# Kernel tuning notes

Measured on AMD Instinct MI355X. Metric: run time of the kernel, lower is better.

## Reference

```python
import jax, jax.numpy as jnp
import numpy as np

B, S, D, H = 8, 1024, 512, 8  # batch, seq_len, d_model (per-head!), num_heads


def setup_inputs() -> dict:
    key = jax.random.key(0)
    ks = jax.random.split(key, 9)
    q_ip = jax.random.normal(ks[0], (B, S, D), dtype=jnp.float32)
    k_ip = jax.random.normal(ks[1], (B, S, D), dtype=jnp.float32)
    v_ip = jax.random.normal(ks[2], (B, S, D), dtype=jnp.float32)
    # float padding-style mask, 1 => masked out (added as mask * -1e9)
    mask = (jax.random.uniform(ks[3], (B, 1, S, S)) < 0.1).astype(jnp.float32)
    scale = 1.0 / np.sqrt(D)  # lecun_normal-ish init scale
    wq = jax.random.normal(ks[4], (D, D * H), dtype=jnp.float32) * scale
    wk = jax.random.normal(ks[5], (D, D * H), dtype=jnp.float32) * scale
    wv = jax.random.normal(ks[6], (D, D * H), dtype=jnp.float32) * scale
    wo = jax.random.normal(ks[7], (D * H, D), dtype=jnp.float32) * (1.0 / np.sqrt(D * H))
    bq = jnp.zeros((D * H,), jnp.float32)
    bk = jnp.zeros((D * H,), jnp.float32)
    bv = jnp.zeros((D * H,), jnp.float32)
    bo = jnp.zeros((D,), jnp.float32)
    return {"v_ip": v_ip, "k_ip": k_ip, "q_ip": q_ip, "mask": mask,
            "wq": wq, "bq": bq, "wk": wk, "bk": bk, "wv": wv, "bv": bv,
            "wo": wo, "bo": bo}


def _split_heads(x, batch, heads, depth):
    # (B, S, H*D) -> (B, H, S, D)
    return x.reshape(batch, -1, heads, depth).transpose(0, 2, 1, 3)


def reference(v_ip, k_ip, q_ip, mask, wq, bq, wk, bk, wv, bv, wo, bo):
    batch = q_ip.shape[0]
    depth = q_ip.shape[-1]          # d_model (= per-head depth in this 'narrow' MHA)
    heads = wq.shape[-1] // depth
    q = _split_heads(q_ip @ wq + bq, batch, heads, depth)  # (B,H,Sq,D)
    k = _split_heads(k_ip @ wk + bk, batch, heads, depth)  # (B,H,Sk,D)
    v = _split_heads(v_ip @ wv + bv, batch, heads, depth)  # (B,H,Sk,D)
    logits = jnp.einsum('bhqd,bhkd->bhqk', q, k) / jnp.sqrt(jnp.float32(depth))
    logits = logits + mask * (-1e9)
    attn = jax.nn.softmax(logits, axis=-1)                  # (B,H,Sq,Sk)
    ctx = jnp.einsum('bhqk,bhkd->bhqd', attn, v)
    ctx = ctx.transpose(0, 2, 1, 3).reshape(batch, -1, heads * depth)
    out = ctx @ wo + bo                                     # (B,Sq,d_model)
    return out, attn
```

## Files before the change

### kernel.cpp

```cpp
#include <hip/hip_runtime.h>
#include <stdint.h>
#include <stddef.h>

typedef _Float16 h16;
typedef __attribute__((ext_vector_type(4))) _Float16 h16x4;
typedef __attribute__((ext_vector_type(8))) _Float16 h16x8;
typedef __attribute__((ext_vector_type(4))) float f32x4;

#define MFMA16(a, b, c) __builtin_amdgcn_mfma_f32_16x16x32_f16((a), (b), (c), 0, 0, 0)

#define NB 8
#define SEQ 1024
#define DEP 512
#define NH 8
#define HD 4096
#define BS 8192

static __device__ __forceinline__ void gload_lds16(const void* g, void* l) {
  __builtin_amdgcn_global_load_lds((__attribute__((address_space(1))) void*)(g),
                                   (__attribute__((address_space(3))) void*)(l),
                                   16, 0, 0);
}

static __device__ __forceinline__ h16 f2h(float f) { return (h16)f; }

__global__ __launch_bounds__(256) void k_conv3(const float* __restrict__ q,
                                               const float* __restrict__ k,
                                               const float* __restrict__ v,
                                               h16* __restrict__ xq, h16* __restrict__ xk,
                                               h16* __restrict__ xv) {
  int z = blockIdx.y;
  const float* in = z == 0 ? q : (z == 1 ? k : v);
  h16* out = z == 0 ? xq : (z == 1 ? xk : xv);
  int i = blockIdx.x * 256 + threadIdx.x;
  float4 f = ((const float4*)in)[i];
  h16x4 o = { f2h(f.x), f2h(f.y), f2h(f.z), f2h(f.w) };
  ((h16x4*)out)[i] = o;
}

__global__ __launch_bounds__(256) void k_maskbits(const float* __restrict__ mask,
                                                  uint32_t* __restrict__ bits) {
  int g = blockIdx.x * 256 + threadIdx.x;
  const float4* mp = (const float4*)mask + (size_t)g * 8;
  uint32_t w = 0;
#pragma unroll
  for (int u = 0; u < 8; ++u) {
    float4 f = mp[u];
    w |= (f.x != 0.f ? 1u : 0u) << (u * 4);
    w |= (f.y != 0.f ? 1u : 0u) << (u * 4 + 1);
    w |= (f.z != 0.f ? 1u : 0u) << (u * 4 + 2);
    w |= (f.w != 0.f ? 1u : 0u) << (u * 4 + 3);
  }
  bits[g] = w;
}

__global__ __launch_bounds__(256) void k_transpose(const float* __restrict__ in,
                                                   h16* __restrict__ out, int R, int C) {
  __shared__ float t[32][33];
  int c0 = blockIdx.x * 32, r0 = blockIdx.y * 32;
  int tx = threadIdx.x & 31, ty = threadIdx.x >> 5;
  for (int p = 0; p < 4; ++p)
    t[ty + p * 8][tx] = in[(size_t)(r0 + ty + p * 8) * C + c0 + tx];
  __syncthreads();
  for (int p = 0; p < 4; ++p)
    out[(size_t)(c0 + ty + p * 8) * R + r0 + tx] = f2h(t[tx][ty + p * 8]);
}

__global__ __launch_bounds__(256) void k_transpose3(const float* __restrict__ wq,
                                                    const float* __restrict__ wk,
                                                    const float* __restrict__ wv,
                                                    h16* __restrict__ oq, h16* __restrict__ ok,
                                                    h16* __restrict__ ov) {
  __shared__ float t[32][33];
  int z = blockIdx.z;
  const float* in = z == 0 ? wq : (z == 1 ? wk : wv);
  h16* out = z == 0 ? oq : (z == 1 ? ok : ov);
  const int R = 512, C = 4096;
  int c0 = blockIdx.x * 32, r0 = blockIdx.y * 32;
  int tx = threadIdx.x & 31, ty = threadIdx.x >> 5;
  for (int p = 0; p < 4; ++p)
    t[ty + p * 8][tx] = in[(size_t)(r0 + ty + p * 8) * C + c0 + tx];
  __syncthreads();
  for (int p = 0; p < 4; ++p)
    out[(size_t)(c0 + ty + p * 8) * R + r0 + tx] = f2h(t[tx][ty + p * 8]);
}

__global__ __launch_bounds__(256) void k_gemm_qkv(
    const h16* __restrict__ xq, const h16* __restrict__ xk, const h16* __restrict__ xv,
    const h16* __restrict__ WqT, const h16* __restrict__ WkT, const h16* __restrict__ WvT,
    const float* __restrict__ bq, const float* __restrict__ bk, const float* __restrict__ bv,
    h16* __restrict__ Qh, h16* __restrict__ Kh, h16* __restrict__ Vt) {
  __shared__ __align__(16) h16 As[128 * 64];
  __shared__ __align__(16) h16 Bs[128 * 64];
  const int z = blockIdx.z;
  const h16* A = z == 0 ? xq : (z == 1 ? xk : xv);
  const h16* Bm = z == 0 ? WqT : (z == 1 ? WkT : WvT);
  const float* bias = z == 0 ? bq : (z == 1 ? bk : bv);
  const int K = 512;
  const int tid = threadIdx.x, lane = tid & 63, wave = tid >> 6;
  const int wm = (wave >> 1) * 64, wn = (wave & 1) * 64;
  const int m0 = blockIdx.y * 128;
  const int n0 = blockIdx.x * 128;

  f32x4 acc[4][4];
  for (int i = 0; i < 4; ++i)
    for (int j = 0; j < 4; ++j) acc[i][j] = (f32x4)0.0f;

  const int lrow = lane >> 3, lcol = (lane & 7) * 8;
  const int fr = lane & 15, qd = lane >> 4;

  for (int k0 = 0; k0 < K; k0 += 64) {
    __syncthreads();
    for (int i = 0; i < 4; ++i) {
      int g = wave * 4 + i;
      int row = g * 8 + lrow;
      gload_lds16(A + (size_t)(m0 + row) * K + k0 + lcol, As + g * 512);
      gload_lds16(Bm + (size_t)(n0 + row) * K + k0 + lcol, Bs + g * 512);
    }
    __syncthreads();
    for (int kk = 0; kk < 64; kk += 32) {
      h16x8 af[4], bf[4];
      for (int i = 0; i < 4; ++i)
        af[i] = *(const h16x8*)(As + (wm + i * 16 + fr) * 64 + kk + qd * 8);
      for (int j = 0; j < 4; ++j)
        bf[j] = *(const h16x8*)(Bs + (wn + j * 16 + fr) * 64 + kk + qd * 8);
      for (int i = 0; i < 4; ++i)
        for (int j = 0; j < 4; ++j) acc[i][j] = MFMA16(af[i], bf[j], acc[i][j]);
    }
  }

  h16* Cnat = z == 0 ? Qh : Kh;
  for (int i = 0; i < 4; ++i)
    for (int j = 0; j < 4; ++j) {
      int mbase = m0 + wm + i * 16 + qd * 4;
      int ncol = n0 + wn + j * 16 + fr;
      float bv2 = bias[ncol];
      if (z < 2) {
        for (int r = 0; r < 4; ++r)
          Cnat[(size_t)(mbase + r) * HD + ncol] = f2h(acc[i][j][r] + bv2);
      } else {
        int bb = mbase >> 10, ss = mbase & 1023;
        int hh = ncol >> 9, dd = ncol & 511;
        size_t addr = ((size_t)((bb * NH + hh) * DEP + dd)) * SEQ + ss;
        h16x4 pk = { f2h(acc[i][j][0] + bv2), f2h(acc[i][j][1] + bv2),
                     f2h(acc[i][j][2] + bv2), f2h(acc[i][j][3] + bv2) };
        *(h16x4*)(Vt + addr) = pk;
      }
    }
}

template <int OUT_MODE>
__global__ __launch_bounds__(256) void k_gemm_nt(const h16* __restrict__ A,
                                                 const h16* __restrict__ Bm,
                                                 const float* __restrict__ bias,
                                                 void* __restrict__ Cout,
                                                 int M, int N, int K, int ldc) {
  __shared__ __align__(16) h16 As[128 * 64];
  __shared__ __align__(16) h16 Bs[128 * 64];
  const int tid = threadIdx.x, lane = tid & 63, wave = tid >> 6;
  const int wm = (wave >> 1) * 64, wn = (wave & 1) * 64;
  const int m0 = blockIdx.y * 128;
  const int n0 = blockIdx.x * 128;

  f32x4 acc[4][4];
  for (int i = 0; i < 4; ++i)
    for (int j = 0; j < 4; ++j) acc[i][j] = (f32x4)0.0f;

  const int lrow = lane >> 3, lcol = (lane & 7) * 8;
  const int fr = lane & 15, qd = lane >> 4;

  for (int k0 = 0; k0 < K; k0 += 64) {
    __syncthreads();
    for (int i = 0; i < 4; ++i) {
      int g = wave * 4 + i;
      int row = g * 8 + lrow;
      gload_lds16(A + (size_t)(m0 + row) * K + k0 + lcol, As + g * 512);
      gload_lds16(Bm + (size_t)(n0 + row) * K + k0 + lcol, Bs + g * 512);
    }
    __syncthreads();
    for (int kk = 0; kk < 64; kk += 32) {
      h16x8 af[4], bf[4];
      for (int i = 0; i < 4; ++i)
        af[i] = *(const h16x8*)(As + (wm + i * 16 + fr) * 64 + kk + qd * 8);
      for (int j = 0; j < 4; ++j)
        bf[j] = *(const h16x8*)(Bs + (wn + j * 16 + fr) * 64 + kk + qd * 8);
      for (int i = 0; i < 4; ++i)
        for (int j = 0; j < 4; ++j) acc[i][j] = MFMA16(af[i], bf[j], acc[i][j]);
    }
  }

  for (int i = 0; i < 4; ++i)
    for (int j = 0; j < 4; ++j) {
      int mbase = m0 + wm + i * 16 + qd * 4;
      int ncol = n0 + wn + j * 16 + fr;
      float bv2 = bias ? bias[ncol] : 0.0f;
      float* Cp = (float*)Cout;
      for (int r = 0; r < 4; ++r)
        Cp[(size_t)(mbase + r) * ldc + ncol] = acc[i][j][r] + bv2;
    }
}

#define TQ 64
#define QS_LD 520
#define OFF_KS 66560
#define PA_C64 4616
#define OFF_RED 147712
#define CS_LD 536
#define SMEM_ATTN (OFF_RED + 2048)

__global__ __launch_bounds__(512, 2) void k_attn(const h16* __restrict__ Q,
                                                 const h16* __restrict__ Km,
                                                 const uint32_t* __restrict__ bits,
                                                 const h16* __restrict__ Vtg,
                                                 float* __restrict__ attn,
                                                 h16* __restrict__ ctx) {
  extern __shared__ __align__(16) char smem[];
  h16* Qs = (h16*)smem;
  h16* Ks = (h16*)(smem + OFF_KS);
  h16* Pa = (h16*)smem;
  h16* Cs = (h16*)smem;
  float* red = (float*)(smem + OFF_RED);

  const int tid = threadIdx.x, lane = tid & 63, wave = tid >> 6;
  const int qt = blockIdx.x, hh = blockIdx.y, b = blockIdx.z;
  const int q0 = qt * TQ;
  const int fr = lane & 15, qd = lane >> 4;
  const int ncol0 = wave * 128;
  const int bh = b * NH + hh;

  {
    const h16* Qg = Q + (size_t)(b * SEQ + q0) * HD + hh * DEP;
    for (int it = 0; it < 8; ++it) {
      int g = tid + it * 512;
      int row = g >> 6, c8 = g & 63;
      *(h16x8*)(Qs + row * QS_LD + c8 * 8) = *(const h16x8*)(Qg + (size_t)row * HD + c8 * 8);
    }
  }

  f32x4 acc[4][8];
  for (int i = 0; i < 4; ++i)
    for (int j = 0; j < 8; ++j) acc[i][j] = (f32x4)0.0f;

  for (int kc = 0; kc < 512; kc += 32) {
    __syncthreads();
    for (int c = 0; c < 8; ++c) {
      int nbase = wave * 128 + c * 16;
      int n = nbase + (lane >> 2);
      int s = lane & 3;
      int sp = (s - (n >> 1)) & 3;
      gload_lds16(Km + (size_t)(b * SEQ + n) * HD + hh * DEP + kc + sp * 8,
                  Ks + nbase * 32);
    }
    __syncthreads();
    h16x8 af[4];
    for (int i = 0; i < 4; ++i)
      af[i] = *(const h16x8*)(Qs + (i * 16 + fr) * QS_LD + kc + qd * 8);
#pragma unroll
    for (int j = 0; j < 8; ++j) {
      int n = ncol0 + j * 16 + fr;
      int slot = (qd + (n >> 1)) & 3;
      h16x8 bf = *(const h16x8*)(Ks + n * 32 + slot * 8);
      for (int i = 0; i < 4; ++i) acc[i][j] = MFMA16(af[i], bf, acc[i][j]);
    }
  }

  const float scale = 0.044194173824159216f;
  const uint32_t* bitp = bits + (size_t)(b * SEQ + q0) * 32 + wave * 4;
  float rmax[4][4];
#pragma unroll
  for (int i = 0; i < 4; ++i) {
    uint4 mwi[4];
    for (int r = 0; r < 4; ++r)
      mwi[r] = *(const uint4*)(bitp + (size_t)(i * 16 + qd * 4 + r) * 32);
    for (int r = 0; r < 4; ++r) rmax[i][r] = -3.4e38f;
#pragma unroll
    for (int j = 0; j < 8; ++j)
      for (int r = 0; r < 4; ++r) {
        uint32_t ww = (j >> 1) == 0 ? mwi[r].x
                    : (j >> 1) == 1 ? mwi[r].y
                    : (j >> 1) == 2 ? mwi[r].z : mwi[r].w;
        uint32_t m = (ww >> (fr + ((j & 1) << 4))) & 1u;
        float v = acc[i][j][r] * scale + (m ? -1e9f : 0.0f);
        acc[i][j][r] = v;
        rmax[i][r] = fmaxf(rmax[i][r], v);
      }
  }
  for (int i = 0; i < 4; ++i)
    for (int r = 0; r < 4; ++r)
      for (int off = 1; off < 16; off <<= 1)
        rmax[i][r] = fmaxf(rmax[i][r], __shfl_xor(rmax[i][r], off, 64));
  __syncthreads();
  if (fr == 0)
    for (int i = 0; i < 4; ++i)
      for (int r = 0; r < 4; ++r) red[wave * TQ + i * 16 + qd * 4 + r] = rmax[i][r];
  __syncthreads();
  float gmax[4][4];
  for (int i = 0; i < 4; ++i)
    for (int r = 0; r < 4; ++r) {
      int lr = i * 16 + qd * 4 + r;
      float m = red[lr];
      for (int w = 1; w < 8; ++w) m = fmaxf(m, red[w * TQ + lr]);
      gmax[i][r] = m;
    }
  __syncthreads();

  float rsum[4][4];
  for (int i = 0; i < 4; ++i)
    for (int r = 0; r < 4; ++r) rsum[i][r] = 0.f;
  for (int i = 0; i < 4; ++i)
    for (int j = 0; j < 8; ++j)
      for (int r = 0; r < 4; ++r) {
        float e = __expf(acc[i][j][r] - gmax[i][r]);
        acc[i][j][r] = e;
        rsum[i][r] += e;
      }
  for (int i = 0; i < 4; ++i)
    for (int r = 0; r < 4; ++r)
      for (int off = 1; off < 16; off <<= 1)
        rsum[i][r] += __shfl_xor(rsum[i][r], off, 64);
  if (fr == 0)
    for (int i = 0; i < 4; ++i)
      for (int r = 0; r < 4; ++r) red[wave * TQ + i * 16 + qd * 4 + r] = rsum[i][r];
  __syncthreads();

  for (int i = 0; i < 4; ++i)
    for (int r = 0; r < 4; ++r) {
      int lr = i * 16 + qd * 4 + r;
      float tot = 0.f;
      for (int w = 0; w < 8; ++w) tot += red[w * TQ + lr];
      float inv = 1.0f / tot;
#pragma unroll
      for (int j = 0; j < 8; ++j) {
        int c64 = wave * 2 + (j >> 2);
        int coff = ((j & 3) << 4) + fr;
        Pa[c64 * PA_C64 + lr * 72 + coff] = f2h(acc[i][j][r] * inv);
      }
    }
  __syncthreads();

  {
    int row = tid >> 3, p = tid & 7;
    float* ab = attn + (size_t)bh * (SEQ * (size_t)SEQ) + (size_t)(q0 + row) * SEQ;
#pragma unroll
    for (int cc = 0; cc < 4; ++cc) {
      int c2 = p * 4 + cc;
      const h16* src = Pa + (c2 >> 1) * PA_C64 + row * 72 + (c2 & 1) * 32;
      float* dst = ab + c2 * 32;
#pragma unroll
      for (int u = 0; u < 4; ++u) {
        h16x8 hv = *(const h16x8*)(src + u * 8);
        float4 lo = { (float)hv[0], (float)hv[1], (float)hv[2], (float)hv[3] };
        float4 hi = { (float)hv[4], (float)hv[5], (float)hv[6], (float)hv[7] };
        *(float4*)(dst + u * 8) = lo;
        *(float4*)(dst + u * 8 + 4) = hi;
      }
    }
  }

  const int d0 = wave * 64;
  const h16* Vb = Vtg + (size_t)bh * (DEP * (size_t)SEQ);
  f32x4 acc2[4][4];
  for (int i = 0; i < 4; ++i)
    for (int j = 0; j < 4; ++j) acc2[i][j] = (f32x4)0.0f;

  h16x8 bfn[4];
#pragma unroll
  for (int j = 0; j < 4; ++j)
    bfn[j] = *(const h16x8*)(Vb + (size_t)(d0 + j * 16 + fr) * SEQ + qd * 8);
  for (int c2 = 0; c2 < 32; ++c2) {
    h16x8 bf[4];
#pragma unroll
    for (int j = 0; j < 4; ++j) bf[j] = bfn[j];
    if (c2 < 31) {
#pragma unroll
      for (int j = 0; j < 4; ++j)
        bfn[j] = *(const h16x8*)(Vb + (size_t)(d0 + j * 16 + fr) * SEQ + (c2 + 1) * 32 + qd * 8);
    }
    h16x8 af2[4];
#pragma unroll
    for (int i = 0; i < 4; ++i)
      af2[i] = *(const h16x8*)(Pa + (c2 >> 1) * PA_C64 + (i * 16 + fr) * 72 + (c2 & 1) * 32 + qd * 8);
    for (int i = 0; i < 4; ++i)
      for (int j = 0; j < 4; ++j) acc2[i][j] = MFMA16(af2[i], bf[j], acc2[i][j]);
  }

  __syncthreads();
  for (int i = 0; i < 4; ++i)
    for (int j = 0; j < 4; ++j)
      for (int r = 0; r < 4; ++r)
        Cs[(i * 16 + qd * 4 + r) * CS_LD + d0 + j * 16 + fr] = f2h(acc2[i][j][r]);
  __syncthreads();
  {
    int row = tid >> 3, p = tid & 7;
    h16* cg = ctx + (size_t)(b * SEQ + q0 + row) * HD + hh * DEP + p * 64;
#pragma unroll
    for (int u = 0; u < 8; ++u)
      *(h16x8*)(cg + u * 8) = *(const h16x8*)(Cs + row * CS_LD + p * 64 + u * 8);
  }
}

extern "C" void kernel_launch(void* const* d_in, const int* in_sizes, int n_in,
                              void* d_out, int out_size, void* d_ws, size_t ws_size,
                              hipStream_t stream) {
  const float* v_ip = (const float*)d_in[0];
  const float* k_ip = (const float*)d_in[1];
  const float* q_ip = (const float*)d_in[2];
  const float* mask = (const float*)d_in[3];
  const float* wq = (const float*)d_in[4];
  const float* bq = (const float*)d_in[5];
  const float* wk = (const float*)d_in[6];
  const float* bk = (const float*)d_in[7];
  const float* wv = (const float*)d_in[8];
  const float* bv = (const float*)d_in[9];
  const float* wo = (const float*)d_in[10];
  const float* bo = (const float*)d_in[11];

  char* ws = (char*)d_ws;
  h16* Qh  = (h16*)(ws + (size_t)0);
  h16* Kh  = (h16*)(ws + (size_t)67108864);
  h16* Vt  = (h16*)(ws + (size_t)134217728);
  h16* xq  = (h16*)(ws + (size_t)201326592);
  h16* xk  = (h16*)(ws + (size_t)209715200);
  h16* xv  = (h16*)(ws + (size_t)218103808);
  h16* WqT = (h16*)(ws + (size_t)226492416);
  h16* WkT = (h16*)(ws + (size_t)230686720);
  h16* WvT = (h16*)(ws + (size_t)234881024);
  h16* WoT = (h16*)(ws + (size_t)239075328);
  uint32_t* bits = (uint32_t*)xq;
  h16* ctx = Qh;

  float* out = (float*)d_out;
  float* attn = out + (size_t)BS * DEP;

  hipFuncSetAttribute((const void*)k_attn,
                      hipFuncAttributeMaxDynamicSharedMemorySize, SMEM_ATTN);

  k_conv3<<<dim3(4096, 3), 256, 0, stream>>>(q_ip, k_ip, v_ip, xq, xk, xv);
  k_transpose3<<<dim3(128, 16, 3), 256, 0, stream>>>(wq, wk, wv, WqT, WkT, WvT);
  k_transpose<<<dim3(16, 128), 256, 0, stream>>>(wo, WoT, 4096, 512);
  k_gemm_qkv<<<dim3(32, 64, 3), 256, 0, stream>>>(xq, xk, xv, WqT, WkT, WvT,
                                                  bq, bk, bv, Qh, Kh, Vt);
  k_maskbits<<<1024, 256, 0, stream>>>(mask, bits);
  k_attn<<<dim3(SEQ / TQ, NH, NB), 512, SMEM_ATTN, stream>>>(Qh, Kh, bits, Vt, attn, ctx);
  k_gemm_nt<2><<<dim3(4, 64), 256, 0, stream>>>(ctx, WoT, bo, out, 8192, 512, 4096, 512);
}
```

Baseline: 1.034 ms.

## Halve attention query tile to 32 rows and read Q directly from global

The attention kernel's query tile shrinks from 64 to 32 rows, which halves accumulator registers and shared memory and raises the launch bound to 4 blocks per CU. Q is no longer staged in LDS; each wave loads its MFMA A fragments straight from global memory on every K chunk. The attn and ctx write-back loops are re-indexed to use 16 threads per row with coalesced stores. In exchange, twice as many blocks each re-stream the full K and V for their head, and every wave makes redundant uncached-pattern global Q loads.

```diff
diff --git a/kernel.cpp b/kernel.cpp
--- a/kernel.cpp
+++ b/kernel.cpp
@@ -200,23 +200,20 @@
     }
 }
 
-#define TQ 64
-#define QS_LD 520
-#define OFF_KS 66560
-#define PA_C64 4616
-#define OFF_RED 147712
+#define TQ 32
+#define PA_C64 2312
+#define OFF_RED 73984
 #define CS_LD 536
-#define SMEM_ATTN (OFF_RED + 2048)
-
-__global__ __launch_bounds__(512, 2) void k_attn(const h16* __restrict__ Q,
+#define SMEM_ATTN (OFF_RED + 1024)
+
+__global__ __launch_bounds__(512, 4) void k_attn(const h16* __restrict__ Q,
                                                  const h16* __restrict__ Km,
                                                  const uint32_t* __restrict__ bits,
                                                  const h16* __restrict__ Vtg,
                                                  float* __restrict__ attn,
                                                  h16* __restrict__ ctx) {
   extern __shared__ __align__(16) char smem[];
-  h16* Qs = (h16*)smem;
-  h16* Ks = (h16*)(smem + OFF_KS);
+  h16* Ks = (h16*)smem;
   h16* Pa = (h16*)smem;
   h16* Cs = (h16*)smem;
   float* red = (float*)(smem + OFF_RED);
@@ -228,17 +225,10 @@
   const int ncol0 = wave * 128;
   const int bh = b * NH + hh;
 
-  {
-    const h16* Qg = Q + (size_t)(b * SEQ + q0) * HD + hh * DEP;
-    for (int it = 0; it < 8; ++it) {
-      int g = tid + it * 512;
-      int row = g >> 6, c8 = g & 63;
-      *(h16x8*)(Qs + row * QS_LD + c8 * 8) = *(const h16x8*)(Qg + (size_t)row * HD + c8 * 8);
-    }
-  }
-
-  f32x4 acc[4][8];
-  for (int i = 0; i < 4; ++i)
+  const h16* Qg = Q + (size_t)(b * SEQ + q0) * HD + hh * DEP;
+
+  f32x4 acc[2][8];
+  for (int i = 0; i < 2; ++i)
     for (int j = 0; j < 8; ++j) acc[i][j] = (f32x4)0.0f;
 
   for (int kc = 0; kc < 512; kc += 32) {
@@ -251,24 +241,25 @@
       gload_lds16(Km + (size_t)(b * SEQ + n) * HD + hh * DEP + kc + sp * 8,
                   Ks + nbase * 32);
     }
-    __syncthreads();
-    h16x8 af[4];
-    for (int i = 0; i < 4; ++i)
-      af[i] = *(const h16x8*)(Qs + (i * 16 + fr) * QS_LD + kc + qd * 8);
+    h16x8 af[2];
+#pragma unroll
+    for (int i = 0; i < 2; ++i)
+      af[i] = *(const h16x8*)(Qg + (size_t)(i * 16 + fr) * HD + kc + qd * 8);
+    __syncthreads();
 #pragma unroll
     for (int j = 0; j < 8; ++j) {
       int n = ncol0 + j * 16 + fr;
       int slot = (qd + (n >> 1)) & 3;
       h16x8 bf = *(const h16x8*)(Ks + n * 32 + slot * 8);
-      for (int i = 0; i < 4; ++i) acc[i][j] = MFMA16(af[i], bf, acc[i][j]);
+      for (int i = 0; i < 2; ++i) acc[i][j] = MFMA16(af[i], bf, acc[i][j]);
     }
   }
 
   const float scale = 0.044194173824159216f;
   const uint32_t* bitp = bits + (size_t)(b * SEQ + q0) * 32 + wave * 4;
-  float rmax[4][4];
-#pragma unroll
-  for (int i = 0; i < 4; ++i) {
+  float rmax[2][4];
+#pragma unroll
+  for (int i = 0; i < 2; ++i) {
     uint4 mwi[4];
     for (int r = 0; r < 4; ++r)
       mwi[r] = *(const uint4*)(bitp + (size_t)(i * 16 + qd * 4 + r) * 32);
@@ -285,17 +276,17 @@
         rmax[i][r] = fmaxf(rmax[i][r], v);
       }
   }
-  for (int i = 0; i < 4; ++i)
+  for (int i = 0; i < 2; ++i)
     for (int r = 0; r < 4; ++r)
       for (int off = 1; off < 16; off <<= 1)
         rmax[i][r] = fmaxf(rmax[i][r], __shfl_xor(rmax[i][r], off, 64));
   __syncthreads();
   if (fr == 0)
-    for (int i = 0; i < 4; ++i)
+    for (int i = 0; i < 2; ++i)
       for (int r = 0; r < 4; ++r) red[wave * TQ + i * 16 + qd * 4 + r] = rmax[i][r];
   __syncthreads();
-  float gmax[4][4];
-  for (int i = 0; i < 4; ++i)
+  float gmax[2][4];
+  for (int i = 0; i < 2; ++i)
     for (int r = 0; r < 4; ++r) {
       int lr = i * 16 + qd * 4 + r;
       float m = red[lr];
@@ -304,26 +295,26 @@
     }
   __syncthreads();
 
-  float rsum[4][4];
-  for (int i = 0; i < 4; ++i)
+  float rsum[2][4];
+  for (int i = 0; i < 2; ++i)
     for (int r = 0; r < 4; ++r) rsum[i][r] = 0.f;
-  for (int i = 0; i < 4; ++i)
+  for (int i = 0; i < 2; ++i)
     for (int j = 0; j < 8; ++j)
       for (int r = 0; r < 4; ++r) {
         float e = __expf(acc[i][j][r] - gmax[i][r]);
         acc[i][j][r] = e;
         rsum[i][r] += e;
       }
-  for (int i = 0; i < 4; ++i)
+  for (int i = 0; i < 2; ++i)
     for (int r = 0; r < 4; ++r)
       for (int off = 1; off < 16; off <<= 1)
         rsum[i][r] += __shfl_xor(rsum[i][r], off, 64);
   if (fr == 0)
-    for (int i = 0; i < 4; ++i)
+    for (int i = 0; i < 2; ++i)
       for (int r = 0; r < 4; ++r) red[wave * TQ + i * 16 + qd * 4 + r] = rsum[i][r];
   __syncthreads();
 
-  for (int i = 0; i < 4; ++i)
+  for (int i = 0; i < 2; ++i)
     for (int r = 0; r < 4; ++r) {
       int lr = i * 16 + qd * 4 + r;
       float tot = 0.f;
@@ -339,28 +330,21 @@
   __syncthreads();
 
   {
-    int row = tid >> 3, p = tid & 7;
+    int row = tid >> 4, p = tid & 15;
     float* ab = attn + (size_t)bh * (SEQ * (size_t)SEQ) + (size_t)(q0 + row) * SEQ;
 #pragma unroll
-    for (int cc = 0; cc < 4; ++cc) {
-      int c2 = p * 4 + cc;
-      const h16* src = Pa + (c2 >> 1) * PA_C64 + row * 72 + (c2 & 1) * 32;
-      float* dst = ab + c2 * 32;
-#pragma unroll
-      for (int u = 0; u < 4; ++u) {
-        h16x8 hv = *(const h16x8*)(src + u * 8);
-        float4 lo = { (float)hv[0], (float)hv[1], (float)hv[2], (float)hv[3] };
-        float4 hi = { (float)hv[4], (float)hv[5], (float)hv[6], (float)hv[7] };
-        *(float4*)(dst + u * 8) = lo;
-        *(float4*)(dst + u * 8 + 4) = hi;
-      }
+    for (int u = 0; u < 16; ++u) {
+      const h16* src = Pa + u * PA_C64 + row * 72 + p * 4;
+      h16x4 hv = *(const h16x4*)src;
+      float4 f = { (float)hv[0], (float)hv[1], (float)hv[2], (float)hv[3] };
+      *(float4*)(ab + u * 64 + p * 4) = f;
     }
   }
 
   const int d0 = wave * 64;
   const h16* Vb = Vtg + (size_t)bh * (DEP * (size_t)SEQ);
-  f32x4 acc2[4][4];
-  for (int i = 0; i < 4; ++i)
+  f32x4 acc2[2][4];
+  for (int i = 0; i < 2; ++i)
     for (int j = 0; j < 4; ++j) acc2[i][j] = (f32x4)0.0f;
 
   h16x8 bfn[4];
@@ -376,26 +360,26 @@
       for (int j = 0; j < 4; ++j)
         bfn[j] = *(const h16x8*)(Vb + (size_t)(d0 + j * 16 + fr) * SEQ + (c2 + 1) * 32 + qd * 8);
     }
-    h16x8 af2[4];
-#pragma unroll
-    for (int i = 0; i < 4; ++i)
+    h16x8 af2[2];
+#pragma unroll
+    for (int i = 0; i < 2; ++i)
       af2[i] = *(const h16x8*)(Pa + (c2 >> 1) * PA_C64 + (i * 16 + fr) * 72 + (c2 & 1) * 32 + qd * 8);
-    for (int i = 0; i < 4; ++i)
+    for (int i = 0; i < 2; ++i)
       for (int j = 0; j < 4; ++j) acc2[i][j] = MFMA16(af2[i], bf[j], acc2[i][j]);
   }
 
   __syncthreads();
-  for (int i = 0; i < 4; ++i)
+  for (int i = 0; i < 2; ++i)
     for (int j = 0; j < 4; ++j)
       for (int r = 0; r < 4; ++r)
         Cs[(i * 16 + qd * 4 + r) * CS_LD + d0 + j * 16 + fr] = f2h(acc2[i][j][r]);
   __syncthreads();
   {
-    int row = tid >> 3, p = tid & 7;
-    h16* cg = ctx + (size_t)(b * SEQ + q0 + row) * HD + hh * DEP + p * 64;
-#pragma unroll
-    for (int u = 0; u < 8; ++u)
-      *(h16x8*)(cg + u * 8) = *(const h16x8*)(Cs + row * CS_LD + p * 64 + u * 8);
+    int row = tid >> 4, p = tid & 15;
+    h16* cg = ctx + (size_t)(b * SEQ + q0 + row) * HD + hh * DEP;
+#pragma unroll
+    for (int u = 0; u < 4; ++u)
+      *(h16x8*)(cg + u * 128 + p * 8) = *(const h16x8*)(Cs + row * CS_LD + u * 128 + p * 8);
   }
 }
 
```

New measurement: 1.099 ms. 1.06x slower.

## Restructure attention kernel to 1024 threads with double-buffered K and XCD-aware grid

Applied to the files above, without the earlier changes.

The attention kernel now runs 16 waves per block, each owning 64 key columns instead of 128. K tiles are double-buffered in LDS so the next chunk's global-to-LDS load overlaps the current MFMAs. Q fragments are read directly from global memory instead of being staged in LDS. A 1D grid is remapped so that blocks sharing the same batch-head land on the same XCD, aiming at better L2 reuse of K and V. The changes trade fewer accumulator registers per thread for more waves and more uncached Q reads. The launch bounds of (1024,4) may be unachievable given the LDS size.

```diff
diff --git a/kernel.cpp b/kernel.cpp
--- a/kernel.cpp
+++ b/kernel.cpp
@@ -201,84 +201,85 @@
 }
 
 #define TQ 64
-#define QS_LD 520
-#define OFF_KS 66560
+#define OFF_KS1 65536
 #define PA_C64 4616
 #define OFF_RED 147712
 #define CS_LD 536
-#define SMEM_ATTN (OFF_RED + 2048)
-
-__global__ __launch_bounds__(512, 2) void k_attn(const h16* __restrict__ Q,
-                                                 const h16* __restrict__ Km,
-                                                 const uint32_t* __restrict__ bits,
-                                                 const h16* __restrict__ Vtg,
-                                                 float* __restrict__ attn,
-                                                 h16* __restrict__ ctx) {
+#define SMEM_ATTN (OFF_RED + 4096)
+
+__global__ __launch_bounds__(1024, 4) void k_attn(const h16* __restrict__ Q,
+                                                  const h16* __restrict__ Km,
+                                                  const uint32_t* __restrict__ bits,
+                                                  const h16* __restrict__ Vtg,
+                                                  float* __restrict__ attn,
+                                                  h16* __restrict__ ctx) {
   extern __shared__ __align__(16) char smem[];
-  h16* Qs = (h16*)smem;
-  h16* Ks = (h16*)(smem + OFF_KS);
+  h16* Ks0 = (h16*)smem;
+  h16* Ks1 = (h16*)(smem + OFF_KS1);
   h16* Pa = (h16*)smem;
   h16* Cs = (h16*)smem;
   float* red = (float*)(smem + OFF_RED);
 
   const int tid = threadIdx.x, lane = tid & 63, wave = tid >> 6;
-  const int qt = blockIdx.x, hh = blockIdx.y, b = blockIdx.z;
+  const int wgid = blockIdx.x;
+  const int xcd = wgid & 7, g = wgid >> 3;
+  const int qt = g & 15;
+  const int bh = ((g >> 4) << 3) + xcd;
+  const int b = bh >> 3, hh = bh & 7;
   const int q0 = qt * TQ;
   const int fr = lane & 15, qd = lane >> 4;
-  const int ncol0 = wave * 128;
-  const int bh = b * NH + hh;
-
-  {
-    const h16* Qg = Q + (size_t)(b * SEQ + q0) * HD + hh * DEP;
-    for (int it = 0; it < 8; ++it) {
-      int g = tid + it * 512;
-      int row = g >> 6, c8 = g & 63;
-      *(h16x8*)(Qs + row * QS_LD + c8 * 8) = *(const h16x8*)(Qg + (size_t)row * HD + c8 * 8);
-    }
-  }
-
-  f32x4 acc[4][8];
-  for (int i = 0; i < 4; ++i)
-    for (int j = 0; j < 8; ++j) acc[i][j] = (f32x4)0.0f;
-
+
+  const h16* Qg = Q + (size_t)(b * SEQ + q0) * HD + hh * DEP;
+  const h16* Kg = Km + (size_t)(b * SEQ) * HD + hh * DEP;
+
+  f32x4 acc[4][4];
+  for (int i = 0; i < 4; ++i)
+    for (int j = 0; j < 4; ++j) acc[i][j] = (f32x4)0.0f;
+
+#define STAGE_K(Kb, kc)                                                      \
+  do {                                                                       \
+    for (int c = 0; c < 4; ++c) {                                            \
+      int nbase = wave * 64 + c * 16;                                        \
+      int n = nbase + (lane >> 2);                                           \
+      int s = lane & 3;                                                      \
+      int sp = (s - (n >> 1)) & 3;                                           \
+      gload_lds16(Kg + (size_t)n * HD + (kc) + sp * 8, (Kb) + nbase * 32);   \
+    }                                                                        \
+  } while (0)
+
+  STAGE_K(Ks0, 0);
+  int cur = 0;
   for (int kc = 0; kc < 512; kc += 32) {
     __syncthreads();
-    for (int c = 0; c < 8; ++c) {
-      int nbase = wave * 128 + c * 16;
-      int n = nbase + (lane >> 2);
-      int s = lane & 3;
-      int sp = (s - (n >> 1)) & 3;
-      gload_lds16(Km + (size_t)(b * SEQ + n) * HD + hh * DEP + kc + sp * 8,
-                  Ks + nbase * 32);
-    }
-    __syncthreads();
+    if (kc + 32 < 512) STAGE_K(cur ? Ks0 : Ks1, kc + 32);
     h16x8 af[4];
+#pragma unroll
     for (int i = 0; i < 4; ++i)
-      af[i] = *(const h16x8*)(Qs + (i * 16 + fr) * QS_LD + kc + qd * 8);
-#pragma unroll
-    for (int j = 0; j < 8; ++j) {
-      int n = ncol0 + j * 16 + fr;
+      af[i] = *(const h16x8*)(Qg + (size_t)(i * 16 + fr) * HD + kc + qd * 8);
+    const h16* Kb = cur ? Ks1 : Ks0;
+#pragma unroll
+    for (int j = 0; j < 4; ++j) {
+      int n = wave * 64 + j * 16 + fr;
       int slot = (qd + (n >> 1)) & 3;
-      h16x8 bf = *(const h16x8*)(Ks + n * 32 + slot * 8);
+      h16x8 bf = *(const h16x8*)(Kb + n * 32 + slot * 8);
       for (int i = 0; i < 4; ++i) acc[i][j] = MFMA16(af[i], bf, acc[i][j]);
     }
+    cur ^= 1;
   }
 
   const float scale = 0.044194173824159216f;
-  const uint32_t* bitp = bits + (size_t)(b * SEQ + q0) * 32 + wave * 4;
+  const uint32_t* bitp = bits + (size_t)(b * SEQ + q0) * 32 + wave * 2;
   float rmax[4][4];
 #pragma unroll
   for (int i = 0; i < 4; ++i) {
-    uint4 mwi[4];
+    uint2 mwi[4];
     for (int r = 0; r < 4; ++r)
-      mwi[r] = *(const uint4*)(bitp + (size_t)(i * 16 + qd * 4 + r) * 32);
+      mwi[r] = *(const uint2*)(bitp + (size_t)(i * 16 + qd * 4 + r) * 32);
     for (int r = 0; r < 4; ++r) rmax[i][r] = -3.4e38f;
 #pragma unroll
-    for (int j = 0; j < 8; ++j)
+    for (int j = 0; j < 4; ++j)
       for (int r = 0; r < 4; ++r) {
-        uint32_t ww = (j >> 1) == 0 ? mwi[r].x
-                    : (j >> 1) == 1 ? mwi[r].y
-                    : (j >> 1) == 2 ? mwi[r].z : mwi[r].w;
+        uint32_t ww = (j >> 1) == 0 ? mwi[r].x : mwi[r].y;
         uint32_t m = (ww >> (fr + ((j & 1) << 4))) & 1u;
         float v = acc[i][j][r] * scale + (m ? -1e9f : 0.0f);
         acc[i][j][r] = v;
@@ -299,7 +300,7 @@
     for (int r = 0; r < 4; ++r) {
       int lr = i * 16 + qd * 4 + r;
       float m = red[lr];
-      for (int w = 1; w < 8; ++w) m = fmaxf(m, red[w * TQ + lr]);
+      for (int w = 1; w < 16; ++w) m = fmaxf(m, red[w * TQ + lr]);
       gmax[i][r] = m;
     }
   __syncthreads();
@@ -308,7 +309,7 @@
   for (int i = 0; i < 4; ++i)
     for (int r = 0; r < 4; ++r) rsum[i][r] = 0.f;
   for (int i = 0; i < 4; ++i)
-    for (int j = 0; j < 8; ++j)
+    for (int j = 0; j < 4; ++j)
       for (int r = 0; r < 4; ++r) {
         float e = __expf(acc[i][j][r] - gmax[i][r]);
         acc[i][j][r] = e;
@@ -327,53 +328,43 @@
     for (int r = 0; r < 4; ++r) {
       int lr = i * 16 + qd * 4 + r;
       float tot = 0.f;
-      for (int w = 0; w < 8; ++w) tot += red[w * TQ + lr];
+      for (int w = 0; w < 16; ++w) tot += red[w * TQ + lr];
       float inv = 1.0f / tot;
 #pragma unroll
-      for (int j = 0; j < 8; ++j) {
-        int c64 = wave * 2 + (j >> 2);
-        int coff = ((j & 3) << 4) + fr;
-        Pa[c64 * PA_C64 + lr * 72 + coff] = f2h(acc[i][j][r] * inv);
-      }
+      for (int j = 0; j < 4; ++j)
+        Pa[wave * PA_C64 + lr * 72 + j * 16 + fr] = f2h(acc[i][j][r] * inv);
     }
   __syncthreads();
 
   {
-    int row = tid >> 3, p = tid & 7;
+    int row = tid >> 4, p = tid & 15;
     float* ab = attn + (size_t)bh * (SEQ * (size_t)SEQ) + (size_t)(q0 + row) * SEQ;
 #pragma unroll
-    for (int cc = 0; cc < 4; ++cc) {
-      int c2 = p * 4 + cc;
-      const h16* src = Pa + (c2 >> 1) * PA_C64 + row * 72 + (c2 & 1) * 32;
-      float* dst = ab + c2 * 32;
-#pragma unroll
-      for (int u = 0; u < 4; ++u) {
-        h16x8 hv = *(const h16x8*)(src + u * 8);
-        float4 lo = { (float)hv[0], (float)hv[1], (float)hv[2], (float)hv[3] };
-        float4 hi = { (float)hv[4], (float)hv[5], (float)hv[6], (float)hv[7] };
-        *(float4*)(dst + u * 8) = lo;
-        *(float4*)(dst + u * 8 + 4) = hi;
-      }
-    }
-  }
-
-  const int d0 = wave * 64;
+    for (int u = 0; u < 16; ++u) {
+      const h16* src = Pa + u * PA_C64 + row * 72 + p * 4;
+      h16x4 hv = *(const h16x4*)src;
+      float4 f = { (float)hv[0], (float)hv[1], (float)hv[2], (float)hv[3] };
+      *(float4*)(ab + u * 64 + p * 4) = f;
+    }
+  }
+
+  const int d0 = wave * 32;
   const h16* Vb = Vtg + (size_t)bh * (DEP * (size_t)SEQ);
-  f32x4 acc2[4][4];
-  for (int i = 0; i < 4; ++i)
-    for (int j = 0; j < 4; ++j) acc2[i][j] = (f32x4)0.0f;
-
-  h16x8 bfn[4];
-#pragma unroll
-  for (int j = 0; j < 4; ++j)
+  f32x4 acc2[4][2];
+  for (int i = 0; i < 4; ++i)
+    for (int j = 0; j < 2; ++j) acc2[i][j] = (f32x4)0.0f;
+
+  h16x8 bfn[2];
+#pragma unroll
+  for (int j = 0; j < 2; ++j)
     bfn[j] = *(const h16x8*)(Vb + (size_t)(d0 + j * 16 + fr) * SEQ + qd * 8);
   for (int c2 = 0; c2 < 32; ++c2) {
-    h16x8 bf[4];
-#pragma unroll
-    for (int j = 0; j < 4; ++j) bf[j] = bfn[j];
+    h16x8 bf[2];
+#pragma unroll
+    for (int j = 0; j < 2; ++j) bf[j] = bfn[j];
     if (c2 < 31) {
 #pragma unroll
-      for (int j = 0; j < 4; ++j)
+      for (int j = 0; j < 2; ++j)
         bfn[j] = *(const h16x8*)(Vb + (size_t)(d0 + j * 16 + fr) * SEQ + (c2 + 1) * 32 + qd * 8);
     }
     h16x8 af2[4];
@@ -381,21 +372,21 @@
     for (int i = 0; i < 4; ++i)
       af2[i] = *(const h16x8*)(Pa + (c2 >> 1) * PA_C64 + (i * 16 + fr) * 72 + (c2 & 1) * 32 + qd * 8);
     for (int i = 0; i < 4; ++i)
-      for (int j = 0; j < 4; ++j) acc2[i][j] = MFMA16(af2[i], bf[j], acc2[i][j]);
-  }
-
-  __syncthreads();
-  for (int i = 0; i < 4; ++i)
-    for (int j = 0; j < 4; ++j)
+      for (int j = 0; j < 2; ++j) acc2[i][j] = MFMA16(af2[i], bf[j], acc2[i][j]);
+  }
+
+  __syncthreads();
+  for (int i = 0; i < 4; ++i)
+    for (int j = 0; j < 2; ++j)
       for (int r = 0; r < 4; ++r)
         Cs[(i * 16 + qd * 4 + r) * CS_LD + d0 + j * 16 + fr] = f2h(acc2[i][j][r]);
   __syncthreads();
   {
-    int row = tid >> 3, p = tid & 7;
-    h16* cg = ctx + (size_t)(b * SEQ + q0 + row) * HD + hh * DEP + p * 64;
-#pragma unroll
-    for (int u = 0; u < 8; ++u)
-      *(h16x8*)(cg + u * 8) = *(const h16x8*)(Cs + row * CS_LD + p * 64 + u * 8);
+    int row = tid >> 4, p = tid & 15;
+    h16* cg = ctx + (size_t)(b * SEQ + q0 + row) * HD + hh * DEP;
+#pragma unroll
+    for (int u = 0; u < 4; ++u)
+      *(h16x8*)(cg + u * 128 + p * 8) = *(const h16x8*)(Cs + row * CS_LD + u * 128 + p * 8);
   }
 }
 
@@ -441,6 +432,6 @@
   k_gemm_qkv<<<dim3(32, 64, 3), 256, 0, stream>>>(xq, xk, xv, WqT, WkT, WvT,
                                                   bq, bk, bv, Qh, Kh, Vt);
   k_maskbits<<<1024, 256, 0, stream>>>(mask, bits);
-  k_attn<<<dim3(SEQ / TQ, NH, NB), 512, SMEM_ATTN, stream>>>(Qh, Kh, bits, Vt, attn, ctx);
+  k_attn<<<dim3(1024), 1024, SMEM_ATTN, stream>>>(Qh, Kh, bits, Vt, attn, ctx);
   k_gemm_nt<2><<<dim3(4, 64), 256, 0, stream>>>(ctx, WoT, bo, out, 8192, 512, 4096, 512);
 }
```

Result: slower. 1.142 ms (+10.4%).

## Double-buffer K tiles in attention QK loop and remap workgroups per XCD

Applied to the files above, without the earlier changes.

The QK^T loop now double-buffers K tiles in LDS and prefetches the next tile with global_load_lds while computing on the current one, using explicit vmcnt waits and barriers instead of two full syncthreads per step. Q fragments are read straight from global into registers with one-step prefetch, so the Q staging in LDS goes away. The PV loop deepens its V register prefetch to two stages. The grid is flattened to 1D and remapped so all query tiles of a batch-head land on the same XCD, aiming for better L2 reuse of K and V. This costs more registers and relies on hand-tuned wait counts being correct.

```diff
diff --git a/kernel.cpp b/kernel.cpp
--- a/kernel.cpp
+++ b/kernel.cpp
@@ -201,8 +201,7 @@
 }
 
 #define TQ 64
-#define QS_LD 520
-#define OFF_KS 66560
+#define OFF_KS1 65536
 #define PA_C64 4616
 #define OFF_RED 147712
 #define CS_LD 536
@@ -215,53 +214,72 @@
                                                  float* __restrict__ attn,
                                                  h16* __restrict__ ctx) {
   extern __shared__ __align__(16) char smem[];
-  h16* Qs = (h16*)smem;
-  h16* Ks = (h16*)(smem + OFF_KS);
+  h16* Ks0 = (h16*)smem;
+  h16* Ks1 = (h16*)(smem + OFF_KS1);
   h16* Pa = (h16*)smem;
   h16* Cs = (h16*)smem;
   float* red = (float*)(smem + OFF_RED);
 
   const int tid = threadIdx.x, lane = tid & 63, wave = tid >> 6;
-  const int qt = blockIdx.x, hh = blockIdx.y, b = blockIdx.z;
+  const int wgid = blockIdx.x;
+  const int xcd = wgid & 7, g = wgid >> 3;
+  const int qt = g & 15;
+  const int bh = ((g >> 4) << 3) + xcd;
+  const int b = bh >> 3, hh = bh & 7;
   const int q0 = qt * TQ;
   const int fr = lane & 15, qd = lane >> 4;
   const int ncol0 = wave * 128;
-  const int bh = b * NH + hh;
-
-  {
-    const h16* Qg = Q + (size_t)(b * SEQ + q0) * HD + hh * DEP;
-    for (int it = 0; it < 8; ++it) {
-      int g = tid + it * 512;
-      int row = g >> 6, c8 = g & 63;
-      *(h16x8*)(Qs + row * QS_LD + c8 * 8) = *(const h16x8*)(Qg + (size_t)row * HD + c8 * 8);
-    }
-  }
+
+  const h16* Qg = Q + (size_t)(b * SEQ + q0) * HD + hh * DEP;
+  const h16* Kg = Km + (size_t)(b * SEQ) * HD + hh * DEP;
 
   f32x4 acc[4][8];
   for (int i = 0; i < 4; ++i)
     for (int j = 0; j < 8; ++j) acc[i][j] = (f32x4)0.0f;
 
+#define STAGE_K(Kb, kc)                                                      \
+  do {                                                                       \
+    for (int c = 0; c < 8; ++c) {                                            \
+      int nbase = wave * 128 + c * 16;                                       \
+      int n = nbase + (lane >> 2);                                           \
+      int s = lane & 3;                                                      \
+      int sp = (s - (n >> 1)) & 3;                                           \
+      gload_lds16(Kg + (size_t)n * HD + (kc) + sp * 8, (Kb) + nbase * 32);   \
+    }                                                                        \
+  } while (0)
+
+  h16x8 afc[4], afn[4];
+#pragma unroll
+  for (int i = 0; i < 4; ++i)
+    afc[i] = *(const h16x8*)(Qg + (size_t)(i * 16 + fr) * HD + qd * 8);
+  STAGE_K(Ks0, 0);
+
+  int cur = 0;
   for (int kc = 0; kc < 512; kc += 32) {
-    __syncthreads();
-    for (int c = 0; c < 8; ++c) {
-      int nbase = wave * 128 + c * 16;
-      int n = nbase + (lane >> 2);
-      int s = lane & 3;
-      int sp = (s - (n >> 1)) & 3;
-      gload_lds16(Km + (size_t)(b * SEQ + n) * HD + hh * DEP + kc + sp * 8,
-                  Ks + nbase * 32);
-    }
-    __syncthreads();
-    h16x8 af[4];
-    for (int i = 0; i < 4; ++i)
-      af[i] = *(const h16x8*)(Qs + (i * 16 + fr) * QS_LD + kc + qd * 8);
+    if (kc + 32 < 512) {
+#pragma unroll
+      for (int i = 0; i < 4; ++i)
+        afn[i] = *(const h16x8*)(Qg + (size_t)(i * 16 + fr) * HD + (kc + 32) + qd * 8);
+      STAGE_K(cur ? Ks0 : Ks1, kc + 32);
+      asm volatile("s_waitcnt vmcnt(12)" ::: "memory");
+    } else {
+      asm volatile("s_waitcnt vmcnt(0)" ::: "memory");
+    }
+    __builtin_amdgcn_s_barrier();
+    __builtin_amdgcn_sched_barrier(0);
+    const h16* Kb = cur ? Ks1 : Ks0;
 #pragma unroll
     for (int j = 0; j < 8; ++j) {
       int n = ncol0 + j * 16 + fr;
       int slot = (qd + (n >> 1)) & 3;
-      h16x8 bf = *(const h16x8*)(Ks + n * 32 + slot * 8);
-      for (int i = 0; i < 4; ++i) acc[i][j] = MFMA16(af[i], bf, acc[i][j]);
-    }
+      h16x8 bf = *(const h16x8*)(Kb + n * 32 + slot * 8);
+      for (int i = 0; i < 4; ++i) acc[i][j] = MFMA16(afc[i], bf, acc[i][j]);
+    }
+    __builtin_amdgcn_sched_barrier(0);
+    __builtin_amdgcn_s_barrier();
+#pragma unroll
+    for (int i = 0; i < 4; ++i) afc[i] = afn[i];
+    cur ^= 1;
   }
 
   const float scale = 0.044194173824159216f;
@@ -363,25 +381,30 @@
   for (int i = 0; i < 4; ++i)
     for (int j = 0; j < 4; ++j) acc2[i][j] = (f32x4)0.0f;
 
-  h16x8 bfn[4];
+  h16x8 bf0[4], bf1[4];
 #pragma unroll
   for (int j = 0; j < 4; ++j)
-    bfn[j] = *(const h16x8*)(Vb + (size_t)(d0 + j * 16 + fr) * SEQ + qd * 8);
+    bf0[j] = *(const h16x8*)(Vb + (size_t)(d0 + j * 16 + fr) * SEQ + qd * 8);
+#pragma unroll
+  for (int j = 0; j < 4; ++j)
+    bf1[j] = *(const h16x8*)(Vb + (size_t)(d0 + j * 16 + fr) * SEQ + 32 + qd * 8);
   for (int c2 = 0; c2 < 32; ++c2) {
-    h16x8 bf[4];
-#pragma unroll
-    for (int j = 0; j < 4; ++j) bf[j] = bfn[j];
-    if (c2 < 31) {
+    h16x8 bfu[4];
+#pragma unroll
+    for (int j = 0; j < 4; ++j) bfu[j] = bf0[j];
+#pragma unroll
+    for (int j = 0; j < 4; ++j) bf0[j] = bf1[j];
+    if (c2 + 2 < 32) {
 #pragma unroll
       for (int j = 0; j < 4; ++j)
-        bfn[j] = *(const h16x8*)(Vb + (size_t)(d0 + j * 16 + fr) * SEQ + (c2 + 1) * 32 + qd * 8);
+        bf1[j] = *(const h16x8*)(Vb + (size_t)(d0 + j * 16 + fr) * SEQ + (c2 + 2) * 32 + qd * 8);
     }
     h16x8 af2[4];
 #pragma unroll
     for (int i = 0; i < 4; ++i)
       af2[i] = *(const h16x8*)(Pa + (c2 >> 1) * PA_C64 + (i * 16 + fr) * 72 + (c2 & 1) * 32 + qd * 8);
     for (int i = 0; i < 4; ++i)
-      for (int j = 0; j < 4; ++j) acc2[i][j] = MFMA16(af2[i], bf[j], acc2[i][j]);
+      for (int j = 0; j < 4; ++j) acc2[i][j] = MFMA16(af2[i], bfu[j], acc2[i][j]);
   }
 
   __syncthreads();
@@ -441,6 +464,6 @@
   k_gemm_qkv<<<dim3(32, 64, 3), 256, 0, stream>>>(xq, xk, xv, WqT, WkT, WvT,
                                                   bq, bk, bv, Qh, Kh, Vt);
   k_maskbits<<<1024, 256, 0, stream>>>(mask, bits);
-  k_attn<<<dim3(SEQ / TQ, NH, NB), 512, SMEM_ATTN, stream>>>(Qh, Kh, bits, Vt, attn, ctx);
+  k_attn<<<dim3(1024), 512, SMEM_ATTN, stream>>>(Qh, Kh, bits, Vt, attn, ctx);
   k_gemm_nt<2><<<dim3(4, 64), 256, 0, stream>>>(ctx, WoT, bo, out, 8192, 512, 4096, 512);
 }
```

Result: slower. 1.063 ms (+2.8%).
